# Kernel optimization log

Measured on AMD Instinct MI355X. Metric: run time of the kernel, lower is better.

Reference implementation:

```python
import jax, jax.numpy as jnp
import numpy as np

N_NODES = 100000
N_HYPER = 20000
N_EDGES = 1600000
D = 128


def layer_norm(x, gamma, beta, eps=1e-5):
    mu = jnp.mean(x, axis=-1, keepdims=True)
    var = jnp.mean(jnp.square(x - mu), axis=-1, keepdims=True)
    return (x - mu) * jax.lax.rsqrt(var + eps) * gamma + beta


def setup_inputs() -> dict:
    key = jax.random.key(0)
    ks = jax.random.split(key, 12)
    s = 1.0 / np.sqrt(D)
    s4 = 1.0 / np.sqrt(4 * D)
    return {
        "h": jax.random.normal(ks[0], (N_NODES, D), jnp.float32),
        "src": jax.random.randint(ks[1], (N_EDGES,), 0, N_NODES),
        "dst": jax.random.randint(ks[2], (N_EDGES,), 0, N_HYPER),
        # node->hyperedge GraphConv
        "W1": jax.random.normal(ks[3], (D, D), jnp.float32) * s,
        "b1": jnp.zeros((D,), jnp.float32),
        # hyperedge->node GraphConv
        "W2": jax.random.normal(ks[4], (D, D), jnp.float32) * s,
        "b2": jnp.zeros((D,), jnp.float32),
        # FFN
        "W3": jax.random.normal(ks[5], (D, 4 * D), jnp.float32) * s,
        "b3": jnp.zeros((4 * D,), jnp.float32),
        "W4": jax.random.normal(ks[6], (4 * D, D), jnp.float32) * s4,
        "b4": jnp.zeros((D,), jnp.float32),
        # LayerNorms
        "gamma1": jnp.ones((D,), jnp.float32),
        "beta1": jnp.zeros((D,), jnp.float32),
        "gamma2": jnp.ones((D,), jnp.float32),
        "beta2": jnp.zeros((D,), jnp.float32),
    }


def reference(h, src, dst, W1, b1, W2, b2, W3, b3, W4, b4,
              gamma1, beta1, gamma2, beta2):
    ones_e = jnp.ones((N_EDGES,), h.dtype)
    # symmetric GraphConv norms (DGL norm='both', degrees clamped to >= 1)
    deg_node = jnp.maximum(jax.ops.segment_sum(ones_e, src, N_NODES), 1.0)
    deg_he = jnp.maximum(jax.ops.segment_sum(ones_e, dst, N_HYPER), 1.0)
    cn = jax.lax.rsqrt(deg_node)[:, None]  # [N_NODES,1]
    ch = jax.lax.rsqrt(deg_he)[:, None]    # [N_HYPER,1]

    # node -> hyperedge: h_hyper = D_he^{-1/2} A^T D_node^{-1/2} h W1 + b1
    msg = (h * cn)[src]                                  # [E, D]
    h_hyper = jax.ops.segment_sum(msg, dst, N_HYPER) * ch
    h_hyper = h_hyper @ W1 + b1                          # [N_HYPER, D]

    # hyperedge -> node on reversed graph (same norms, swapped roles)
    msg2 = (h_hyper * ch)[dst]                           # [E, D]
    h_node = jax.ops.segment_sum(msg2, src, N_NODES) * cn
    h_node = h_node @ W2 + b2                            # [N_NODES, D]

    # residual + LN, FFN + residual + LN (dropout = identity in eval)
    h1 = layer_norm(h + h_node, gamma1, beta1)
    ffn = jax.nn.relu(h1 @ W3 + b3) @ W4 + b4
    return layer_norm(h1 + ffn, gamma2, beta2)
```

## Files before the change

kernel.cpp:

```cpp
#include <hip/hip_runtime.h>

#define N_NODES 100000
#define N_HYPER 20000
#define N_EDGES 1600000
#define LDW 136
#define LDY 72

#define NB_HE 79
#define NB_ND 391
#define CHUNK 6250

typedef unsigned short u16;
typedef unsigned int u32;
typedef short bf16x8 __attribute__((ext_vector_type(8)));
typedef float f32x4 __attribute__((ext_vector_type(4)));

__device__ __forceinline__ f32x4 mfma16(bf16x8 a, bf16x8 b, f32x4 c) {
    return __builtin_amdgcn_mfma_f32_16x16x32_bf16(a, b, c, 0, 0, 0);
}
__device__ __forceinline__ u16 f2bf(float f) {
    unsigned u = __float_as_uint(f);
    unsigned r = u + 0x7FFFu + ((u >> 16) & 1u);
    return (u16)(r >> 16);
}
__device__ __forceinline__ void bfu(unsigned v, float& f0, float& f1) {
    f0 = __uint_as_float(v << 16);
    f1 = __uint_as_float(v & 0xFFFF0000u);
}

__global__ __launch_bounds__(256) void k_prep(const float* __restrict__ W1, const float* __restrict__ W2,
                                              const float* __restrict__ W3, const float* __restrict__ W4,
                                              u16* __restrict__ W1t, u16* __restrict__ W2t,
                                              u16* __restrict__ W3t, u16* __restrict__ W4t,
                                              const float* __restrict__ h, u16* __restrict__ h_bf) {
    int i = blockIdx.x * 256 + threadIdx.x;
    if (i < 16384) {
        int k = i & 127, n = i >> 7;
        W1t[n * 128 + k] = f2bf(W1[k * 128 + n]);
        W2t[n * 128 + k] = f2bf(W2[k * 128 + n]);
    }
    if (i < 65536) {
        int k = i & 127, n = i >> 7;
        W3t[n * 128 + k] = f2bf(W3[k * 512 + n]);
        int k4 = i & 511, n4 = i >> 9;
        W4t[n4 * 512 + k4] = f2bf(W4[k4 * 128 + n4]);
    }
    if (i < 3276800) {
        float4 v = ((const float4*)h)[i];
        uint2 st;
        st.x = (u32)f2bf(v.x) | ((u32)f2bf(v.y) << 16);
        st.y = (u32)f2bf(v.z) | ((u32)f2bf(v.w) << 16);
        ((uint2*)h_bf)[i] = st;
    }
}

__global__ __launch_bounds__(256) void k_bin_hist(const int* __restrict__ src, const int* __restrict__ dst,
                                                  int* __restrict__ bkt_he, int* __restrict__ bkt_nd) {
    __shared__ int hh[NB_HE], hn[NB_ND];
    int t = threadIdx.x;
    for (int i = t; i < NB_HE; i += 256) hh[i] = 0;
    for (int i = t; i < NB_ND; i += 256) hn[i] = 0;
    __syncthreads();
    int e0 = blockIdx.x * CHUNK;
    for (int e = e0 + t; e < e0 + CHUNK; e += 256) {
        atomicAdd(&hn[src[e] >> 8], 1);
        atomicAdd(&hh[dst[e] >> 8], 1);
    }
    __syncthreads();
    for (int i = t; i < NB_HE; i += 256) if (hh[i]) atomicAdd(&bkt_he[i], hh[i]);
    for (int i = t; i < NB_ND; i += 256) if (hn[i]) atomicAdd(&bkt_nd[i], hn[i]);
}

__global__ __launch_bounds__(512) void k_bin_scan(int* __restrict__ bkt_he, int* __restrict__ bkt_nd,
                                                  int* __restrict__ start_he, int* __restrict__ start_nd,
                                                  int* __restrict__ ptr_node, int* __restrict__ ptr_he) {
    __shared__ int sc[512];
    int t = threadIdx.x;
    int vhe = (t < NB_HE) ? bkt_he[t] : 0;
    sc[t] = vhe; __syncthreads();
    for (int off = 1; off < 512; off <<= 1) {
        int v = (t >= off) ? sc[t - off] : 0; __syncthreads();
        sc[t] += v; __syncthreads();
    }
    if (t < NB_HE) { int ex = sc[t] - vhe; start_he[t] = ex; bkt_he[t] = ex; }
    if (t == NB_HE - 1) start_he[NB_HE] = sc[t];
    __syncthreads();
    int vnd = (t < NB_ND) ? bkt_nd[t] : 0;
    sc[t] = vnd; __syncthreads();
    for (int off = 1; off < 512; off <<= 1) {
        int v = (t >= off) ? sc[t - off] : 0; __syncthreads();
        sc[t] += v; __syncthreads();
    }
    if (t < NB_ND) { int ex = sc[t] - vnd; start_nd[t] = ex; bkt_nd[t] = ex; }
    if (t == NB_ND - 1) start_nd[NB_ND] = sc[t];
    if (t == 0) { ptr_node[N_NODES] = N_EDGES; ptr_he[N_HYPER] = N_EDGES; }
}

__global__ __launch_bounds__(256) void k_bin_fill(const int* __restrict__ src, const int* __restrict__ dst,
                                                  int* __restrict__ bkt_he, int* __restrict__ bkt_nd,
                                                  u32* __restrict__ bin_he, u32* __restrict__ bin_nd) {
    __shared__ int hh[NB_HE], hn[NB_ND], bh[NB_HE], bn[NB_ND];
    int t = threadIdx.x;
    for (int i = t; i < NB_HE; i += 256) hh[i] = 0;
    for (int i = t; i < NB_ND; i += 256) hn[i] = 0;
    __syncthreads();
    int e0 = blockIdx.x * CHUNK;
    for (int e = e0 + t; e < e0 + CHUNK; e += 256) {
        atomicAdd(&hn[src[e] >> 8], 1);
        atomicAdd(&hh[dst[e] >> 8], 1);
    }
    __syncthreads();
    for (int i = t; i < NB_HE; i += 256) { int c = hh[i]; bh[i] = c ? atomicAdd(&bkt_he[i], c) : 0; }
    for (int i = t; i < NB_ND; i += 256) { int c = hn[i]; bn[i] = c ? atomicAdd(&bkt_nd[i], c) : 0; }
    __syncthreads();
    for (int i = t; i < NB_HE; i += 256) hh[i] = 0;
    for (int i = t; i < NB_ND; i += 256) hn[i] = 0;
    __syncthreads();
    for (int e = e0 + t; e < e0 + CHUNK; e += 256) {
        int s = src[e], d = dst[e];
        int bd = d >> 8, bs_ = s >> 8;
        int ph = bh[bd] + atomicAdd(&hh[bd], 1);
        bin_he[ph] = ((u32)(d & 255) << 24) | (u32)s;
        int pn = bn[bs_] + atomicAdd(&hn[bs_], 1);
        bin_nd[pn] = ((u32)(s & 255) << 24) | (u32)d;
    }
}

__global__ __launch_bounds__(256) void k_deg(const u32* __restrict__ bin_he, const u32* __restrict__ bin_nd,
                                             const int* __restrict__ start_he, const int* __restrict__ start_nd,
                                             int* __restrict__ deg_nd, int* __restrict__ deg_he) {
    __shared__ int cnt[256];
    int t = threadIdx.x, b = blockIdx.x;
    cnt[t] = 0; __syncthreads();
    if (b < NB_HE) {
        int lo = start_he[b], hi = start_he[b + 1];
        for (int j = lo + t; j < hi; j += 256) atomicAdd(&cnt[bin_he[j] >> 24], 1);
        __syncthreads();
        int id = b * 256 + t;
        if (id < N_HYPER) deg_he[id] = cnt[t];
    } else {
        int bb = b - NB_HE;
        int lo = start_nd[bb], hi = start_nd[bb + 1];
        for (int j = lo + t; j < hi; j += 256) atomicAdd(&cnt[bin_nd[j] >> 24], 1);
        __syncthreads();
        int id = bb * 256 + t;
        if (id < N_NODES) deg_nd[id] = cnt[t];
    }
}

__global__ __launch_bounds__(256) void k_scanA(const int* __restrict__ a_node,
                                               const int* __restrict__ a_he,
                                               int* __restrict__ bs) {
    __shared__ int red[256];
    int b = blockIdx.x;
    const int* a; int base, n;
    if (b < 25) { a = a_node; base = b * 4096; n = N_NODES; }
    else        { a = a_he;   base = (b - 25) * 4096; n = N_HYPER; }
    int t = threadIdx.x;
    int lo = base + t * 16;
    int s = 0;
#pragma unroll
    for (int i = 0; i < 16; ++i) {
        int idx = lo + i;
        if (idx < n) s += a[idx];
    }
    red[t] = s;
    __syncthreads();
    for (int off = 128; off > 0; off >>= 1) {
        if (t < off) red[t] += red[t + off];
        __syncthreads();
    }
    if (t == 0) bs[b] = red[0];
}

__global__ void k_scanB(int* __restrict__ bs) {
    int t = threadIdx.x;
    if (t == 0) {
        int run = 0;
        for (int i = 0; i < 25; ++i) { int v = bs[i]; bs[i] = run; run += v; }
    } else if (t == 1) {
        int run = 0;
        for (int i = 25; i < 30; ++i) { int v = bs[i]; bs[i] = run; run += v; }
    }
}

__global__ __launch_bounds__(256) void k_scanC(int* __restrict__ a_node, int* __restrict__ a_he,
                                               float* __restrict__ iq_node, float* __restrict__ iq_he,
                                               const int* __restrict__ bs) {
    __shared__ int pre[256];
    int b = blockIdx.x;
    int* a; float* iq; int base, n;
    if (b < 25) { a = a_node; iq = iq_node; base = b * 4096; n = N_NODES; }
    else        { a = a_he;   iq = iq_he;   base = (b - 25) * 4096; n = N_HYPER; }
    int t = threadIdx.x;
    int lo = base + t * 16;
    int loc = 0;
#pragma unroll
    for (int i = 0; i < 16; ++i) { int idx = lo + i; if (idx < n) loc += a[idx]; }
    pre[t] = loc;
    __syncthreads();
    for (int off = 1; off < 256; off <<= 1) {
        int v = (t >= off) ? pre[t - off] : 0;
        __syncthreads();
        pre[t] += v;
        __syncthreads();
    }
    int running = bs[b] + pre[t] - loc;
#pragma unroll
    for (int i = 0; i < 16; ++i) {
        int idx = lo + i;
        if (idx < n) {
            int d = a[idx];
            iq[idx] = rsqrtf((float)(d < 1 ? 1 : d));
            a[idx] = running;
            running += d;
        }
    }
}

__global__ __launch_bounds__(256) void k_fill2(const u32* __restrict__ bin_he, const u32* __restrict__ bin_nd,
                                               const int* __restrict__ start_he, const int* __restrict__ start_nd,
                                               const int* __restrict__ ptr_he, const int* __restrict__ ptr_node,
                                               int* __restrict__ adj_he, int* __restrict__ adj_node) {
    __shared__ int base[256], rk[256];
    int t = threadIdx.x, b = blockIdx.x;
    rk[t] = 0;
    if (b < NB_HE) {
        int id = b * 256 + t;
        base[t] = (id < N_HYPER) ? ptr_he[id] : 0;
        __syncthreads();
        int lo = start_he[b], hi = start_he[b + 1];
        for (int j = lo + t; j < hi; j += 256) {
            u32 v = bin_he[j];
            int lid = v >> 24;
            int pos = base[lid] + atomicAdd(&rk[lid], 1);
            adj_he[pos] = (int)(v & 0xFFFFFFu);
        }
    } else {
        int bb = b - NB_HE;
        int id = bb * 256 + t;
        base[t] = (id < N_NODES) ? ptr_node[id] : 0;
        __syncthreads();
        int lo = start_nd[bb], hi = start_nd[bb + 1];
        for (int j = lo + t; j < hi; j += 256) {
            u32 v = bin_nd[j];
            int lid = v >> 24;
            int pos = base[lid] + atomicAdd(&rk[lid], 1);
            adj_node[pos] = (int)(v & 0xFFFFFFu);
        }
    }
}

__global__ __launch_bounds__(256) void k_gather1(const u16* __restrict__ h_bf,
                                                 const int* __restrict__ adj,
                                                 const int* __restrict__ ptr,
                                                 const float* __restrict__ cn,
                                                 float* __restrict__ acc1) {
    int row = blockIdx.x * 4 + (threadIdx.x >> 6);
    int lane = threadIdx.x & 63;
    int p = lane >> 5, c = lane & 31;
    int start = ptr[row];
    int end = ptr[row + 1];
    const uint2* hp = (const uint2*)h_bf;
    float A0[4] = {0, 0, 0, 0}, A1[4] = {0, 0, 0, 0};
    float f0, f1, f2, f3;
    int j = start;
    for (; j + 3 < end; j += 4) {
        int sA = adj[j + p], sB = adj[j + 2 + p];
        float wA = cn[sA], wB = cn[sB];
        uint2 vA = hp[sA * 32 + c];
        uint2 vB = hp[sB * 32 + c];
        bfu(vA.x, f0, f1); bfu(vA.y, f2, f3);
        A0[0] += f0 * wA; A0[1] += f1 * wA; A0[2] += f2 * wA; A0[3] += f3 * wA;
        bfu(vB.x, f0, f1); bfu(vB.y, f2, f3);
        A1[0] += f0 * wB; A1[1] += f1 * wB; A1[2] += f2 * wB; A1[3] += f3 * wB;
    }
    for (; j + 1 < end; j += 2) {
        int sA = adj[j + p];
        float wA = cn[sA];
        uint2 vA = hp[sA * 32 + c];
        bfu(vA.x, f0, f1); bfu(vA.y, f2, f3);
        A0[0] += f0 * wA; A0[1] += f1 * wA; A0[2] += f2 * wA; A0[3] += f3 * wA;
    }
    if (j < end && p == 0) {
        int sA = adj[j];
        float wA = cn[sA];
        uint2 vA = hp[sA * 32 + c];
        bfu(vA.x, f0, f1); bfu(vA.y, f2, f3);
        A0[0] += f0 * wA; A0[1] += f1 * wA; A0[2] += f2 * wA; A0[3] += f3 * wA;
    }
    float r0 = A0[0] + A1[0], r1 = A0[1] + A1[1], r2 = A0[2] + A1[2], r3 = A0[3] + A1[3];
    r0 += __shfl_xor(r0, 32, 64);
    r1 += __shfl_xor(r1, 32, 64);
    r2 += __shfl_xor(r2, 32, 64);
    r3 += __shfl_xor(r3, 32, 64);
    if (p == 0) {
        float4 o; o.x = r0; o.y = r1; o.z = r2; o.w = r3;
        ((float4*)acc1)[row * 32 + c] = o;
    }
}

__global__ __launch_bounds__(256) void k_gather2(const u16* __restrict__ hh2b,
                                                 const int* __restrict__ adj,
                                                 const int* __restrict__ ptr,
                                                 float* __restrict__ acc2) {
    int row = blockIdx.x * 4 + (threadIdx.x >> 6);
    int lane = threadIdx.x & 63;
    int p = lane >> 5, c = lane & 31;
    int start = ptr[row];
    int end = ptr[row + 1];
    const uint2* hp = (const uint2*)hh2b;
    float A0[4] = {0, 0, 0, 0}, A1[4] = {0, 0, 0, 0};
    float f0, f1, f2, f3;
    int j = start;
    for (; j + 3 < end; j += 4) {
        int dA = adj[j + p], dB = adj[j + 2 + p];
        uint2 vA = hp[dA * 32 + c];
        uint2 vB = hp[dB * 32 + c];
        bfu(vA.x, f0, f1); bfu(vA.y, f2, f3);
        A0[0] += f0; A0[1] += f1; A0[2] += f2; A0[3] += f3;
        bfu(vB.x, f0, f1); bfu(vB.y, f2, f3);
        A1[0] += f0; A1[1] += f1; A1[2] += f2; A1[3] += f3;
    }
    for (; j + 1 < end; j += 2) {
        int dA = adj[j + p];
        uint2 vA = hp[dA * 32 + c];
        bfu(vA.x, f0, f1); bfu(vA.y, f2, f3);
        A0[0] += f0; A0[1] += f1; A0[2] += f2; A0[3] += f3;
    }
    if (j < end && p == 0) {
        int dA = adj[j];
        uint2 vA = hp[dA * 32 + c];
        bfu(vA.x, f0, f1); bfu(vA.y, f2, f3);
        A0[0] += f0; A0[1] += f1; A0[2] += f2; A0[3] += f3;
    }
    float r0 = A0[0] + A1[0], r1 = A0[1] + A1[1], r2 = A0[2] + A1[2], r3 = A0[3] + A1[3];
    r0 += __shfl_xor(r0, 32, 64);
    r1 += __shfl_xor(r1, 32, 64);
    r2 += __shfl_xor(r2, 32, 64);
    r3 += __shfl_xor(r3, 32, 64);
    if (p == 0) {
        float4 o; o.x = r0; o.y = r1; o.z = r2; o.w = r3;
        ((float4*)acc2)[row * 32 + c] = o;
    }
}

__global__ __launch_bounds__(256) void k_gemm1(const float* __restrict__ a, const float* __restrict__ ch,
                                               const u16* __restrict__ W1t,
                                               const float* __restrict__ b1,
                                               u16* __restrict__ hh2b) {
    __shared__ u16 sA[64 * LDW];
    __shared__ u16 sW[128 * LDW];
    int tid = threadIdx.x;
    int r0 = blockIdx.x * 64;
    for (int i = tid; i < 64 * 32; i += 256) {
        int r = i >> 5, c4 = i & 31;
        int row = r0 + r; if (row > N_HYPER - 1) row = N_HYPER - 1;
        float4 v = *(const float4*)(a + row * 128 + c4 * 4);
        float cw = ch[row];
        u16* p = &sA[r * LDW + c4 * 4];
        p[0] = f2bf(v.x * cw); p[1] = f2bf(v.y * cw);
        p[2] = f2bf(v.z * cw); p[3] = f2bf(v.w * cw);
    }
    for (int i = tid; i < 128 * 16; i += 256) {
        int n = i >> 4, c = i & 15;
        *(uint4*)&sW[n * LDW + c * 8] = *(const uint4*)(W1t + n * 128 + c * 8);
    }
    __syncthreads();
    int w = tid >> 6, l15 = tid & 15, quad = (tid & 63) >> 4;
    f32x4 zero = {0.f, 0.f, 0.f, 0.f};
    f32x4 acc[8];
#pragma unroll
    for (int nt = 0; nt < 8; ++nt) acc[nt] = zero;
    int arow = w * 16 + l15;
#pragma unroll
    for (int kt = 0; kt < 4; ++kt) {
        bf16x8 af = *(bf16x8*)&sA[arow * LDW + kt * 32 + quad * 8];
#pragma unroll
        for (int nt = 0; nt < 8; ++nt) {
            bf16x8 bfv = *(bf16x8*)&sW[(nt * 16 + l15) * LDW + kt * 32 + quad * 8];
            acc[nt] = mfma16(af, bfv, acc[nt]);
        }
    }
#pragma unroll
    for (int r = 0; r < 4; ++r) {
        int row = r0 + w * 16 + quad * 4 + r;
        if (row < N_HYPER) {
            float cw = ch[row];
#pragma unroll
            for (int nt = 0; nt < 8; ++nt) {
                int n = nt * 16 + l15;
                hh2b[row * 128 + n] = f2bf((acc[nt][r] + b1[n]) * cw);
            }
        }
    }
}

__global__ __launch_bounds__(256) void k_gemm2_ln(float* a, const float* __restrict__ cn,
                                                  const u16* __restrict__ W2t,
                                                  const float* __restrict__ b2,
                                                  const float* __restrict__ h,
                                                  const float* __restrict__ gamma1,
                                                  const float* __restrict__ beta1) {
    __shared__ u16 sA[64 * LDW];
    __shared__ u16 sW[128 * LDW];
    int tid = threadIdx.x;
    int r0 = blockIdx.x * 64;
    for (int i = tid; i < 64 * 32; i += 256) {
        int r = i >> 5, c4 = i & 31;
        int row = r0 + r; if (row > N_NODES - 1) row = N_NODES - 1;
        float4 v = *(const float4*)(a + row * 128 + c4 * 4);
        float cw = cn[row];
        u16* p = &sA[r * LDW + c4 * 4];
        p[0] = f2bf(v.x * cw); p[1] = f2bf(v.y * cw);
        p[2] = f2bf(v.z * cw); p[3] = f2bf(v.w * cw);
    }
    for (int i = tid; i < 128 * 16; i += 256) {
        int n = i >> 4, c = i & 15;
        *(uint4*)&sW[n * LDW + c * 8] = *(const uint4*)(W2t + n * 128 + c * 8);
    }
    __syncthreads();
    int w = tid >> 6, l15 = tid & 15, quad = (tid & 63) >> 4;
    f32x4 zero = {0.f, 0.f, 0.f, 0.f};
    f32x4 acc[8];
#pragma unroll
    for (int nt = 0; nt < 8; ++nt) acc[nt] = zero;
    int arow = w * 16 + l15;
#pragma unroll
    for (int kt = 0; kt < 4; ++kt) {
        bf16x8 af = *(bf16x8*)&sA[arow * LDW + kt * 32 + quad * 8];
#pragma unroll
        for (int nt = 0; nt < 8; ++nt) {
            bf16x8 bfv = *(bf16x8*)&sW[(nt * 16 + l15) * LDW + kt * 32 + quad * 8];
            acc[nt] = mfma16(af, bfv, acc[nt]);
        }
    }
    float s1[4] = {0, 0, 0, 0}, s2[4] = {0, 0, 0, 0};
#pragma unroll
    for (int r = 0; r < 4; ++r) {
        int row = r0 + w * 16 + quad * 4 + r;
        int rc = row > N_NODES - 1 ? N_NODES - 1 : row;
#pragma unroll
        for (int nt = 0; nt < 8; ++nt) {
            int n = nt * 16 + l15;
            float t = acc[nt][r] + b2[n] + h[rc * 128 + n];
            acc[nt][r] = t;
            s1[r] += t; s2[r] += t * t;
        }
    }
#pragma unroll
    for (int off = 1; off < 16; off <<= 1) {
#pragma unroll
        for (int r = 0; r < 4; ++r) {
            s1[r] += __shfl_xor(s1[r], off, 64);
            s2[r] += __shfl_xor(s2[r], off, 64);
        }
    }
#pragma unroll
    for (int r = 0; r < 4; ++r) {
        int row = r0 + w * 16 + quad * 4 + r;
        if (row < N_NODES) {
            float mu = s1[r] * (1.f / 128.f);
            float var = s2[r] * (1.f / 128.f) - mu * mu;
            float rs = rsqrtf(var + 1e-5f);
#pragma unroll
            for (int nt = 0; nt < 8; ++nt) {
                int n = nt * 16 + l15;
                a[row * 128 + n] = (acc[nt][r] - mu) * rs * gamma1[n] + beta1[n];
            }
        }
    }
}

__global__ __launch_bounds__(256, 3) void k_ffn_ln(const float* __restrict__ h1,
                                                   const u16* __restrict__ W3t,
                                                   const float* __restrict__ b3,
                                                   const u16* __restrict__ W4t,
                                                   const float* __restrict__ b4,
                                                   const float* __restrict__ gamma2,
                                                   const float* __restrict__ beta2,
                                                   float* __restrict__ out) {
    __shared__ u16 sA[64 * LDW];
    __shared__ u16 sY[64 * LDY];
    __shared__ u16 sW[9216];
    int tid = threadIdx.x;
    int r0 = blockIdx.x * 64;
    int s3row = tid >> 2, s3c = tid & 3;
    int s4row = tid >> 1, s4c = tid & 1;

    uint4 wr[4];
#pragma unroll
    for (int j = 0; j < 4; ++j)
        wr[j] = *(const uint4*)(W3t + s3row * 128 + (s3c + 4 * j) * 8);
    for (int i = tid; i < 64 * 32; i += 256) {
        int r = i >> 5, c4 = i & 31;
        int row = r0 + r; if (row > N_NODES - 1) row = N_NODES - 1;
        float4 v = *(const float4*)(h1 + row * 128 + c4 * 4);
        uint2 st;
        st.x = (u32)f2bf(v.x) | ((u32)f2bf(v.y) << 16);
        st.y = (u32)f2bf(v.z) | ((u32)f2bf(v.w) << 16);
        *(uint2*)&sA[r * LDW + c4 * 4] = st;
    }
#pragma unroll
    for (int j = 0; j < 4; ++j)
        *(uint4*)&sW[s3row * LDW + (s3c + 4 * j) * 8] = wr[j];
    __syncthreads();

    int w = tid >> 6, l15 = tid & 15, quad = (tid & 63) >> 4;
    int arow = w * 16 + l15;
    f32x4 zero = {0.f, 0.f, 0.f, 0.f};
    f32x4 acc[8];
#pragma unroll
    for (int nt = 0; nt < 8; ++nt) acc[nt] = zero;

    for (int hc = 0; hc < 8; ++hc) {
        uint4 wr4[4];
#pragma unroll
        for (int j = 0; j < 4; ++j)
            wr4[j] = *(const uint4*)(W4t + s4row * 512 + hc * 64 + (s4c + 2 * j) * 8);
        f32x4 y[4];
#pragma unroll
        for (int nt = 0; nt < 4; ++nt) y[nt] = zero;
#pragma unroll
        for (int kt = 0; kt < 4; ++kt) {
            bf16x8 af = *(bf16x8*)&sA[arow * LDW + kt * 32 + quad * 8];
#pragma unroll
            for (int nt = 0; nt < 4; ++nt) {
                bf16x8 bv = *(bf16x8*)&sW[(nt * 16 + l15) * LDW + kt * 32 + quad * 8];
                y[nt] = mfma16(af, bv, y[nt]);
            }
        }
#pragma unroll
        for (int r = 0; r < 4; ++r) {
            int yrow = w * 16 + quad * 4 + r;
#pragma unroll
            for (int nt = 0; nt < 4; ++nt) {
                int n = nt * 16 + l15;
                float vv = y[nt][r] + b3[hc * 64 + n];
                sY[yrow * LDY + n] = f2bf(vv > 0.f ? vv : 0.f);
            }
        }
        __syncthreads();
#pragma unroll
        for (int j = 0; j < 4; ++j)
            *(uint4*)&sW[s4row * LDY + (s4c + 2 * j) * 8] = wr4[j];
        __syncthreads();
        if (hc < 7) {
#pragma unroll
            for (int j = 0; j < 4; ++j)
                wr[j] = *(const uint4*)(W3t + ((hc + 1) * 64 + s3row) * 128 + (s3c + 4 * j) * 8);
        }
#pragma unroll
        for (int kt = 0; kt < 2; ++kt) {
            bf16x8 ay = *(bf16x8*)&sY[arow * LDY + kt * 32 + quad * 8];
#pragma unroll
            for (int nt = 0; nt < 8; ++nt) {
                bf16x8 bv = *(bf16x8*)&sW[(nt * 16 + l15) * LDY + kt * 32 + quad * 8];
                acc[nt] = mfma16(ay, bv, acc[nt]);
            }
        }
        __syncthreads();
        if (hc < 7) {
#pragma unroll
            for (int j = 0; j < 4; ++j)
                *(uint4*)&sW[s3row * LDW + (s3c + 4 * j) * 8] = wr[j];
            __syncthreads();
        }
    }
    float s1[4] = {0, 0, 0, 0}, s2[4] = {0, 0, 0, 0};
#pragma unroll
    for (int r = 0; r < 4; ++r) {
        int row = r0 + w * 16 + quad * 4 + r;
        int rc = row > N_NODES - 1 ? N_NODES - 1 : row;
#pragma unroll
        for (int nt = 0; nt < 8; ++nt) {
            int n = nt * 16 + l15;
            float t = acc[nt][r] + b4[n] + h1[rc * 128 + n];
            acc[nt][r] = t;
            s1[r] += t; s2[r] += t * t;
        }
    }
#pragma unroll
    for (int off = 1; off < 16; off <<= 1) {
#pragma unroll
        for (int r = 0; r < 4; ++r) {
            s1[r] += __shfl_xor(s1[r], off, 64);
            s2[r] += __shfl_xor(s2[r], off, 64);
        }
    }
#pragma unroll
    for (int r = 0; r < 4; ++r) {
        int row = r0 + w * 16 + quad * 4 + r;
        if (row < N_NODES) {
            float mu = s1[r] * (1.f / 128.f);
            float var = s2[r] * (1.f / 128.f) - mu * mu;
            float rs = rsqrtf(var + 1e-5f);
#pragma unroll
            for (int nt = 0; nt < 8; ++nt) {
                int n = nt * 16 + l15;
                out[row * 128 + n] = (acc[nt][r] - mu) * rs * gamma2[n] + beta2[n];
            }
        }
    }
}

extern "C" void kernel_launch(void* const* d_in, const int* in_sizes, int n_in,
                              void* d_out, int out_size, void* d_ws, size_t ws_size,
                              hipStream_t stream) {
    const float* h      = (const float*)d_in[0];
    const int*   src    = (const int*)d_in[1];
    const int*   dst    = (const int*)d_in[2];
    const float* W1     = (const float*)d_in[3];
    const float* b1     = (const float*)d_in[4];
    const float* W2     = (const float*)d_in[5];
    const float* b2     = (const float*)d_in[6];
    const float* W3     = (const float*)d_in[7];
    const float* b3     = (const float*)d_in[8];
    const float* W4     = (const float*)d_in[9];
    const float* b4     = (const float*)d_in[10];
    const float* gamma1 = (const float*)d_in[11];
    const float* beta1  = (const float*)d_in[12];
    const float* gamma2 = (const float*)d_in[13];
    const float* beta2  = (const float*)d_in[14];
    float* out = (float*)d_out;

    char* ws = (char*)d_ws;
    int*   ptr_node = (int*)(ws + 0);
    int*   ptr_he   = (int*)(ws + 400512);
    int*   adj_he   = (int*)(ws + 481280);
    int*   adj_node = (int*)(ws + 6881280);
    float* cn       = (float*)(ws + 13281280);
    float* ch       = (float*)(ws + 13681280);
    u16*   h_bf     = (u16*)(ws + 24000000);
    u32*   bin_he   = (u32*)(ws + 49600000);
    u32*   bin_nd   = (u32*)(ws + 56000000);
    float* acc1     = (float*)(ws + 62400000);
    int*   bkt_he   = (int*)(ws + 72640000);
    int*   bkt_nd   = (int*)(ws + 72640512);
    int*   start_he = (int*)(ws + 72642560);
    int*   start_nd = (int*)(ws + 72643072);
    int*   bs       = (int*)(ws + 72644864);
    float* acc2     = (float*)(ws + 24000000);
    u16*   hh2b     = (u16*)(ws + 481280);
    u16*   W1t      = (u16*)(ws + 75200000);
    u16*   W2t      = (u16*)(ws + 75232768);
    u16*   W3t      = (u16*)(ws + 75265536);
    u16*   W4t      = (u16*)(ws + 75396608);

    hipMemsetAsync(ws + 72640000, 0, 2560, stream);

    k_prep<<<12800, 256, 0, stream>>>(W1, W2, W3, W4, W1t, W2t, W3t, W4t, h, h_bf);
    k_bin_hist<<<256, 256, 0, stream>>>(src, dst, bkt_he, bkt_nd);
    k_bin_scan<<<1, 512, 0, stream>>>(bkt_he, bkt_nd, start_he, start_nd, ptr_node, ptr_he);
    k_bin_fill<<<256, 256, 0, stream>>>(src, dst, bkt_he, bkt_nd, bin_he, bin_nd);
    k_deg<<<NB_HE + NB_ND, 256, 0, stream>>>(bin_he, bin_nd, start_he, start_nd, ptr_node, ptr_he);
    k_scanA<<<30, 256, 0, stream>>>(ptr_node, ptr_he, bs);
    k_scanB<<<1, 64, 0, stream>>>(bs);
    k_scanC<<<30, 256, 0, stream>>>(ptr_node, ptr_he, cn, ch, bs);
    k_fill2<<<NB_HE + NB_ND, 256, 0, stream>>>(bin_he, bin_nd, start_he, start_nd,
                                               ptr_he, ptr_node, adj_he, adj_node);
    k_gather1<<<5000, 256, 0, stream>>>(h_bf, adj_he, ptr_he, cn, acc1);
    k_gemm1<<<313, 256, 0, stream>>>(acc1, ch, W1t, b1, hh2b);
    k_gather2<<<25000, 256, 0, stream>>>(hh2b, adj_node, ptr_node, acc2);
    k_gemm2_ln<<<1563, 256, 0, stream>>>(acc2, cn, W2t, b2, h, gamma1, beta1);
    k_ffn_ln<<<1563, 256, 0, stream>>>(acc2, W3t, b3, W4t, b4, gamma2, beta2, out);
}
```

Before: 562.1 us.

## Stream FFN weight chunks into swizzled LDS via direct global-to-LDS loads

The FFN kernel now loads W3/W4 chunks with global_load_lds DMA straight into separate double LDS regions instead of staging them through registers. The prep kernel lays the weights out pre-chunked with an XOR swizzle so the LDS reads avoid bank conflicts without padding. The kernel overlaps each next chunk's DMA with the current GEMM using manual waitcnt and barriers. It drops the occupancy hint of 3 blocks per CU and uses more LDS. The hand-written vmcnt accounting is fragile.

```diff
diff --git a/kernel.cpp b/kernel.cpp
--- a/kernel.cpp
+++ b/kernel.cpp
@@ -15,6 +15,9 @@
 typedef short bf16x8 __attribute__((ext_vector_type(8)));
 typedef float f32x4 __attribute__((ext_vector_type(4)));
 
+typedef __attribute__((address_space(3))) unsigned int lds_u32;
+typedef __attribute__((address_space(1))) unsigned int gbl_u32;
+
 __device__ __forceinline__ f32x4 mfma16(bf16x8 a, bf16x8 b, f32x4 c) {
     return __builtin_amdgcn_mfma_f32_16x16x32_bf16(a, b, c, 0, 0, 0);
 }
@@ -26,6 +29,10 @@
 __device__ __forceinline__ void bfu(unsigned v, float& f0, float& f1) {
     f0 = __uint_as_float(v << 16);
     f1 = __uint_as_float(v & 0xFFFF0000u);
+}
+__device__ __forceinline__ void dma16(const u16* g, u16* l) {
+    __builtin_amdgcn_global_load_lds((const gbl_u32*)(const void*)g,
+                                     (lds_u32*)(void*)l, 16, 0, 0);
 }
 
 __global__ __launch_bounds__(256) void k_prep(const float* __restrict__ W1, const float* __restrict__ W2,
@@ -41,9 +48,13 @@
     }
     if (i < 65536) {
         int k = i & 127, n = i >> 7;
-        W3t[n * 128 + k] = f2bf(W3[k * 512 + n]);
+        int hc = n >> 6, nn = n & 63;
+        int g3 = (k >> 3) ^ (nn & 15);
+        W3t[hc * 8192 + nn * 128 + g3 * 8 + (k & 7)] = f2bf(W3[k * 512 + n]);
         int k4 = i & 511, n4 = i >> 9;
-        W4t[n4 * 512 + k4] = f2bf(W4[k4 * 128 + n4]);
+        int hc4 = k4 >> 6, kk = k4 & 63;
+        int g4 = (kk >> 3) ^ (n4 & 7);
+        W4t[hc4 * 8192 + n4 * 64 + g4 * 8 + (kk & 7)] = f2bf(W4[k4 * 128 + n4]);
     }
     if (i < 3276800) {
         float4 v = ((const float4*)h)[i];
@@ -472,26 +483,32 @@
     }
 }
 
-__global__ __launch_bounds__(256, 3) void k_ffn_ln(const float* __restrict__ h1,
-                                                   const u16* __restrict__ W3t,
-                                                   const float* __restrict__ b3,
-                                                   const u16* __restrict__ W4t,
-                                                   const float* __restrict__ b4,
-                                                   const float* __restrict__ gamma2,
-                                                   const float* __restrict__ beta2,
-                                                   float* __restrict__ out) {
-    __shared__ u16 sA[64 * LDW];
-    __shared__ u16 sY[64 * LDY];
-    __shared__ u16 sW[9216];
+__global__ __launch_bounds__(256) void k_ffn_ln(const float* __restrict__ h1,
+                                                const u16* __restrict__ W3s,
+                                                const float* __restrict__ b3,
+                                                const u16* __restrict__ W4s,
+                                                const float* __restrict__ b4,
+                                                const float* __restrict__ gamma2,
+                                                const float* __restrict__ beta2,
+                                                float* __restrict__ out) {
+    __shared__ __align__(16) u16 sA[64 * LDW];
+    __shared__ __align__(16) u16 sY[64 * LDY];
+    __shared__ __align__(16) u16 sW3[8192];
+    __shared__ __align__(16) u16 sW4[8192];
     int tid = threadIdx.x;
+    int w = tid >> 6, lane = tid & 63;
+    int l15 = tid & 15, quad = (tid & 63) >> 4;
     int r0 = blockIdx.x * 64;
-    int s3row = tid >> 2, s3c = tid & 3;
-    int s4row = tid >> 1, s4c = tid & 1;
-
-    uint4 wr[4];
+    int dmaoff = w * 4096 + lane * 16;
+
 #pragma unroll
     for (int j = 0; j < 4; ++j)
-        wr[j] = *(const uint4*)(W3t + s3row * 128 + (s3c + 4 * j) * 8);
+        dma16((const u16*)((const char*)W3s + dmaoff + j * 1024),
+              (u16*)((char*)sW3 + w * 4096 + j * 1024));
+#pragma unroll
+    for (int j = 0; j < 4; ++j)
+        dma16((const u16*)((const char*)W4s + dmaoff + j * 1024),
+              (u16*)((char*)sW4 + w * 4096 + j * 1024));
     for (int i = tid; i < 64 * 32; i += 256) {
         int r = i >> 5, c4 = i & 31;
         int row = r0 + r; if (row > N_NODES - 1) row = N_NODES - 1;
@@ -501,12 +518,10 @@
         st.y = (u32)f2bf(v.z) | ((u32)f2bf(v.w) << 16);
         *(uint2*)&sA[r * LDW + c4 * 4] = st;
     }
-#pragma unroll
-    for (int j = 0; j < 4; ++j)
-        *(uint4*)&sW[s3row * LDW + (s3c + 4 * j) * 8] = wr[j];
-    __syncthreads();
-
-    int w = tid >> 6, l15 = tid & 15, quad = (tid & 63) >> 4;
+    asm volatile("s_waitcnt vmcnt(4) lgkmcnt(0)" ::: "memory");
+    __builtin_amdgcn_s_barrier();
+    __builtin_amdgcn_sched_barrier(0);
+
     int arow = w * 16 + l15;
     f32x4 zero = {0.f, 0.f, 0.f, 0.f};
     f32x4 acc[8];
@@ -514,10 +529,6 @@
     for (int nt = 0; nt < 8; ++nt) acc[nt] = zero;
 
     for (int hc = 0; hc < 8; ++hc) {
-        uint4 wr4[4];
-#pragma unroll
-        for (int j = 0; j < 4; ++j)
-            wr4[j] = *(const uint4*)(W4t + s4row * 512 + hc * 64 + (s4c + 2 * j) * 8);
         f32x4 y[4];
 #pragma unroll
         for (int nt = 0; nt < 4; ++nt) y[nt] = zero;
@@ -526,7 +537,8 @@
             bf16x8 af = *(bf16x8*)&sA[arow * LDW + kt * 32 + quad * 8];
 #pragma unroll
             for (int nt = 0; nt < 4; ++nt) {
-                bf16x8 bv = *(bf16x8*)&sW[(nt * 16 + l15) * LDW + kt * 32 + quad * 8];
+                int r = nt * 16 + l15;
+                bf16x8 bv = *(bf16x8*)&sW3[r * 128 + ((((kt << 2) + quad) ^ l15) << 3)];
                 y[nt] = mfma16(af, bv, y[nt]);
             }
         }
@@ -540,32 +552,41 @@
                 sY[yrow * LDY + n] = f2bf(vv > 0.f ? vv : 0.f);
             }
         }
-        __syncthreads();
-#pragma unroll
-        for (int j = 0; j < 4; ++j)
-            *(uint4*)&sW[s4row * LDY + (s4c + 2 * j) * 8] = wr4[j];
-        __syncthreads();
-        if (hc < 7) {
+        __builtin_amdgcn_s_barrier();
+        __builtin_amdgcn_sched_barrier(0);
+        {
+            const char* g3 = (const char*)W3s + ((hc + 1) & 7) * 16384;
 #pragma unroll
             for (int j = 0; j < 4; ++j)
-                wr[j] = *(const uint4*)(W3t + ((hc + 1) * 64 + s3row) * 128 + (s3c + 4 * j) * 8);
-        }
+                dma16((const u16*)(g3 + dmaoff + j * 1024),
+                      (u16*)((char*)sW3 + w * 4096 + j * 1024));
+        }
+        asm volatile("s_waitcnt vmcnt(4)" ::: "memory");
+        __builtin_amdgcn_s_barrier();
+        __builtin_amdgcn_sched_barrier(0);
 #pragma unroll
         for (int kt = 0; kt < 2; ++kt) {
             bf16x8 ay = *(bf16x8*)&sY[arow * LDY + kt * 32 + quad * 8];
 #pragma unroll
             for (int nt = 0; nt < 8; ++nt) {
-                bf16x8 bv = *(bf16x8*)&sW[(nt * 16 + l15) * LDY + kt * 32 + quad * 8];
+                int rr = nt * 16 + l15;
+                bf16x8 bv = *(bf16x8*)&sW4[rr * 64 + ((((kt << 2) + quad) ^ (l15 & 7)) << 3)];
                 acc[nt] = mfma16(ay, bv, acc[nt]);
             }
         }
-        __syncthreads();
-        if (hc < 7) {
+        if (hc == 7) break;
+        __builtin_amdgcn_s_barrier();
+        __builtin_amdgcn_sched_barrier(0);
+        {
+            const char* g4 = (const char*)W4s + (hc + 1) * 16384;
 #pragma unroll
             for (int j = 0; j < 4; ++j)
-                *(uint4*)&sW[s3row * LDW + (s3c + 4 * j) * 8] = wr[j];
-            __syncthreads();
-        }
+                dma16((const u16*)(g4 + dmaoff + j * 1024),
+                      (u16*)((char*)sW4 + w * 4096 + j * 1024));
+        }
+        asm volatile("s_waitcnt vmcnt(4)" ::: "memory");
+        __builtin_amdgcn_s_barrier();
+        __builtin_amdgcn_sched_barrier(0);
     }
     float s1[4] = {0, 0, 0, 0}, s2[4] = {0, 0, 0, 0};
 #pragma unroll
```

After: 487.1 us. 1.15x faster.
